# Kernel tuning notes

Hardware: AMD Instinct MI355X
Metric: run time of the kernel (lower is better)

Reference implementation:

```python
import jax, jax.numpy as jnp
import numpy as np

B, IN_DIM, OUT_DIM, N_KNOTS = 8192, 1024, 1024, 4


def setup_inputs() -> dict:
    key = jax.random.key(0)
    k_feat, k_phase, k_w = jax.random.split(key, 3)
    feats = jax.random.normal(k_feat, (B, IN_DIM), dtype=jnp.float32)
    phase = jax.random.uniform(k_phase, (B, 1), dtype=jnp.float32)  # phase in [0,1)
    x = jnp.concatenate([feats, phase], axis=1)  # [B, IN_DIM+1]
    bound = np.sqrt(6.0 / (OUT_DIM * IN_DIM))
    weight_knots = jax.random.uniform(
        k_w, (N_KNOTS, OUT_DIM, IN_DIM), dtype=jnp.float32, minval=-bound, maxval=bound)
    bias_knots = jnp.zeros((N_KNOTS, OUT_DIM), dtype=jnp.float32)
    return {"x": x, "weight_knots": weight_knots, "bias_knots": bias_knots}


def _cubic(y, mu):
    # Catmull-Rom cubic blend over the 4 gathered knots, y: [B,4,D], mu: [B,1]
    y0, y1, y2, y3 = y[:, 0], y[:, 1], y[:, 2], y[:, 3]
    return ((-0.5 * y0 + 1.5 * y1 - 1.5 * y2 + 0.5 * y3) * mu * mu * mu
            + (y0 - 2.5 * y1 + 2.0 * y2 - 0.5 * y3) * mu * mu
            + (-0.5 * y0 + 0.5 * y2) * mu + y1)


def reference(x, weight_knots, bias_knots):
    K = weight_knots.shape[0]
    phase = x[:, -1]            # [B]
    feats = x[:, :-1]           # [B, IN_DIM]
    pscale = K * phase
    mu = jnp.mod(pscale, 1.0)[:, None]                       # [B, 1]
    i1 = jnp.mod(pscale.astype(jnp.int32), K)
    idx = jnp.stack([jnp.mod(i1 - 1, K), i1,
                     jnp.mod(i1 + 1, K), jnp.mod(i1 + 2, K)], axis=1)  # [B, 4]
    # Exploit linearity: matvec against each knot matrix once, then blend.
    # Mathematically identical to cubic(W0,..,W3) @ feats + cubic(b0,..,b3).
    yk = jnp.einsum('koi,bi->bko', weight_knots, feats)      # [B, K, OUT]
    y4 = jnp.take_along_axis(yk, idx[:, :, None], axis=1)    # [B, 4, OUT]
    b4 = bias_knots[idx]                                     # [B, 4, OUT]
    res = _cubic(y4 + b4, mu)                                # cubic is linear in y
    return jax.nn.elu(res)
```

## Files before the change

kernel.cpp:

```cpp
#include <hip/hip_runtime.h>
#include <math.h>

#define IN_DIM 1024
#define OUT_DIM 1024
#define NROWS 8192
#define XSTRIDE 1025

typedef __attribute__((ext_vector_type(8))) short bf16x8;
typedef __attribute__((ext_vector_type(4))) float f32x4;

static __device__ __forceinline__ unsigned f2bf(float f) {
  union { float f; unsigned u; } v; v.f = f;
  unsigned u = v.u;
  return (u + 0x7fffu + ((u >> 16) & 1u)) >> 16;
}

__global__ __launch_bounds__(256) void prep_kernel(
    const float* __restrict__ x, const float* __restrict__ W,
    unsigned short* __restrict__ Wb, unsigned short* __restrict__ F,
    float* __restrict__ coef)
{
  const int blk = blockIdx.x;
  if (blk < 2048) {
    const int t = blk * 256 + threadIdx.x;
    const int flat = t * 8;
    const int k = flat >> 20;
    const int o = (flat >> 10) & 1023;
    const int i = flat & 1023;
    const float4 fa = *reinterpret_cast<const float4*>(W + flat);
    const float4 fb = *reinterpret_cast<const float4*>(W + flat + 4);
    uint4 pk;
    pk.x = f2bf(fa.x) | (f2bf(fa.y) << 16);
    pk.y = f2bf(fa.z) | (f2bf(fa.w) << 16);
    pk.z = f2bf(fb.x) | (f2bf(fb.y) << 16);
    pk.w = f2bf(fb.z) | (f2bf(fb.w) << 16);
    const int g = (o & 15) | (k << 4) | ((o >> 4) << 6);
    *reinterpret_cast<uint4*>(Wb + (size_t)g * 1024 + i) = pk;
  } else {
    const int b = blk - 2048;
    const float* xr = x + (size_t)b * XSTRIDE;
    const int i = threadIdx.x * 4;
    ushort4 vv;
    vv.x = (unsigned short)f2bf(xr[i]);     vv.y = (unsigned short)f2bf(xr[i + 1]);
    vv.z = (unsigned short)f2bf(xr[i + 2]); vv.w = (unsigned short)f2bf(xr[i + 3]);
    *reinterpret_cast<ushort4*>(F + (size_t)b * 1024 + i) = vv;
    if (threadIdx.x == 0) {
      const float ps = 4.0f * xr[IN_DIM];
      const int ip = (int)ps;
      const int i1 = ip & 3;
      const float mu = ps - (float)ip;
      const float mu2 = mu * mu, mu3 = mu2 * mu;
      const float c0 = -0.5f * mu3 +        mu2 - 0.5f * mu;
      const float c1 =  1.5f * mu3 - 2.5f * mu2 + 1.0f;
      const float c2 = -1.5f * mu3 + 2.0f * mu2 + 0.5f * mu;
      const float c3 =  0.5f * mu3 - 0.5f * mu2;
      const int d0 = (0-i1)&3, d1 = (1-i1)&3, d2 = (2-i1)&3, d3 = (3-i1)&3;
      float4 cv;
      cv.x = d0==0 ? c1 : d0==1 ? c2 : d0==2 ? c3 : c0;
      cv.y = d1==0 ? c1 : d1==1 ? c2 : d1==2 ? c3 : c0;
      cv.z = d2==0 ? c1 : d2==1 ? c2 : d2==2 ? c3 : c0;
      cv.w = d3==0 ? c1 : d3==1 ? c2 : d3==2 ? c3 : c0;
      *reinterpret_cast<float4*>(coef + (size_t)b * 4) = cv;
    }
  }
}

#define BM 256
#define BN 128
#define BK 64

__global__ __launch_bounds__(256, 2) void gemm_kernel(
    const unsigned short* __restrict__ F,
    const unsigned short* __restrict__ Wb,
    const float* __restrict__ coef,
    const float* __restrict__ bias,
    float* __restrict__ out)
{
  __shared__ unsigned short As[BM * BK];
  __shared__ unsigned short Bs[BN * BK];

  const int tid  = threadIdx.x;
  const int wave = tid >> 6;
  const int lane = tid & 63;
  const int row0  = blockIdx.y * BM;
  const int col0g = blockIdx.x * BN;

  const int srow = tid >> 3;
  const int scc  = tid & 7;
  const int sgc  = (scc ^ (srow & 7)) * 8;

  const int wr = (wave >> 1) * 128;
  const int wc = (wave & 1) * 64;
  const int fm = lane & 15;
  const int fq = lane >> 4;

  f32x4 acc[8][4];
  const f32x4 zero = {0.f, 0.f, 0.f, 0.f};
  #pragma unroll
  for (int a = 0; a < 8; a++)
    #pragma unroll
    for (int b = 0; b < 4; b++)
      acc[a][b] = zero;

  const unsigned short* Abase = F  + (size_t)row0  * 1024;
  const unsigned short* Bbase = Wb + (size_t)col0g * 1024;

  for (int kb = 0; kb < 1024; kb += BK) {
    #pragma unroll
    for (int it = 0; it < 8; it++) {
      const int r = srow + it * 32;
      __builtin_amdgcn_global_load_lds(
          (const __attribute__((address_space(1))) void*)(Abase + (size_t)r * 1024 + kb + sgc),
          (__attribute__((address_space(3))) void*)(As + r * BK + scc * 8), 16, 0, 0);
    }
    #pragma unroll
    for (int it = 0; it < 4; it++) {
      const int r = srow + it * 32;
      __builtin_amdgcn_global_load_lds(
          (const __attribute__((address_space(1))) void*)(Bbase + (size_t)r * 1024 + kb + sgc),
          (__attribute__((address_space(3))) void*)(Bs + r * BK + scc * 8), 16, 0, 0);
    }
    __syncthreads();

    #pragma unroll
    for (int kk = 0; kk < BK; kk += 32) {
      bf16x8 af[8], bfr[4];
      #pragma unroll
      for (int mi = 0; mi < 8; mi++) {
        const int r  = wr + mi * 16 + fm;
        const int lc = ((kk >> 3) + fq) ^ (fm & 7);
        af[mi] = *reinterpret_cast<const bf16x8*>(As + r * BK + lc * 8);
      }
      #pragma unroll
      for (int ni = 0; ni < 4; ni++) {
        const int r  = wc + ni * 16 + fm;
        const int lc = ((kk >> 3) + fq) ^ (fm & 7);
        bfr[ni] = *reinterpret_cast<const bf16x8*>(Bs + r * BK + lc * 8);
      }
      #pragma unroll
      for (int mi = 0; mi < 8; mi++)
        #pragma unroll
        for (int ni = 0; ni < 4; ni++)
          acc[mi][ni] = __builtin_amdgcn_mfma_f32_16x16x32_bf16(
              af[mi], bfr[ni], acc[mi][ni], 0, 0, 0);
    }
    __syncthreads();
  }

  const int o = fm + 16 * (2 * blockIdx.x + (wave & 1));
  const float b0 = bias[o];
  const float b1 = bias[OUT_DIM + o];
  const float b2 = bias[2 * OUT_DIM + o];
  const float b3 = bias[3 * OUT_DIM + o];
  #pragma unroll
  for (int mi = 0; mi < 8; mi++) {
    #pragma unroll
    for (int r = 0; r < 4; r++) {
      const int rloc = wr + mi * 16 + (fq << 2) + r;
      const float4 c = *reinterpret_cast<const float4*>(coef + (size_t)(row0 + rloc) * 4);
      float v = c.x * (acc[mi][0][r] + b0)
              + c.y * (acc[mi][1][r] + b1)
              + c.z * (acc[mi][2][r] + b2)
              + c.w * (acc[mi][3][r] + b3);
      const float e = __expf(v) - 1.0f;
      v = (v > 0.0f) ? v : e;
      out[(size_t)(row0 + rloc) * OUT_DIM + o] = v;
    }
  }
}

extern "C" void kernel_launch(void* const* d_in, const int* in_sizes, int n_in,
                              void* d_out, int out_size, void* d_ws, size_t ws_size,
                              hipStream_t stream) {
  const float* x  = (const float*)d_in[0];
  const float* wk = (const float*)d_in[1];
  const float* bk = (const float*)d_in[2];
  float* out = (float*)d_out;

  char* ws = (char*)d_ws;
  unsigned short* Wb = (unsigned short*)ws;
  unsigned short* F  = (unsigned short*)(ws + (8u << 20));
  float* coef        = (float*)(ws + (24u << 20));

  hipLaunchKernelGGL(prep_kernel, dim3(2048 + NROWS), dim3(256), 0, stream,
                     x, wk, Wb, F, coef);
  hipLaunchKernelGGL(gemm_kernel, dim3(4096 / BN, NROWS / BM), dim3(256), 0, stream,
                     F, Wb, coef, bk, out);
}
```

Before: 156.3 us.

## Switch GEMM to 32x32x16 bf16 MFMA with matching weight interleave

Replaces the 16x16x32 MFMA tiling with 32x32x16 MFMA instructions. Each wave now owns 64 rows by the full 128-column block, and the four knots of 32 outputs are interleaved per 32-column group. The weight prep layout changes from 16-output groups to 32-output groups so the knot blend stays within one lane's registers. The aim is fewer LDS fragment loads per MFMA and higher per-instruction throughput, at the cost of different register pressure and epilogue indexing.

```diff
diff --git a/kernel.cpp b/kernel.cpp
--- a/kernel.cpp
+++ b/kernel.cpp
@@ -7,7 +7,7 @@
 #define XSTRIDE 1025
 
 typedef __attribute__((ext_vector_type(8))) short bf16x8;
-typedef __attribute__((ext_vector_type(4))) float f32x4;
+typedef __attribute__((ext_vector_type(16))) float f32x16;
 
 static __device__ __forceinline__ unsigned f2bf(float f) {
   union { float f; unsigned u; } v; v.f = f;
@@ -34,7 +34,7 @@
     pk.y = f2bf(fa.z) | (f2bf(fa.w) << 16);
     pk.z = f2bf(fb.x) | (f2bf(fb.y) << 16);
     pk.w = f2bf(fb.z) | (f2bf(fb.w) << 16);
-    const int g = (o & 15) | (k << 4) | ((o >> 4) << 6);
+    const int g = (o & 31) | (k << 5) | ((o >> 5) << 7);
     *reinterpret_cast<uint4*>(Wb + (size_t)g * 1024 + i) = pk;
   } else {
     const int b = blk - 2048;
@@ -89,18 +89,16 @@
   const int scc  = tid & 7;
   const int sgc  = (scc ^ (srow & 7)) * 8;
 
-  const int wr = (wave >> 1) * 128;
-  const int wc = (wave & 1) * 64;
-  const int fm = lane & 15;
-  const int fq = lane >> 4;
+  const int wr = wave * 64;
+  const int lm = lane & 31;
+  const int hi = lane >> 5;
 
-  f32x4 acc[8][4];
-  const f32x4 zero = {0.f, 0.f, 0.f, 0.f};
+  f32x16 acc[2][4];
   #pragma unroll
-  for (int a = 0; a < 8; a++)
+  for (int a = 0; a < 2; a++)
     #pragma unroll
     for (int b = 0; b < 4; b++)
-      acc[a][b] = zero;
+      acc[a][b] = (f32x16)(0.0f);
 
   const unsigned short* Abase = F  + (size_t)row0  * 1024;
   const unsigned short* Bbase = Wb + (size_t)col0g * 1024;
@@ -123,45 +121,40 @@
     __syncthreads();
 
     #pragma unroll
-    for (int kk = 0; kk < BK; kk += 32) {
-      bf16x8 af[8], bfr[4];
+    for (int ks = 0; ks < 4; ks++) {
+      const int lc = ((2 * ks + hi) ^ (lm & 7)) * 8;
+      bf16x8 a[2], b[4];
       #pragma unroll
-      for (int mi = 0; mi < 8; mi++) {
-        const int r  = wr + mi * 16 + fm;
-        const int lc = ((kk >> 3) + fq) ^ (fm & 7);
-        af[mi] = *reinterpret_cast<const bf16x8*>(As + r * BK + lc * 8);
-      }
+      for (int mi = 0; mi < 2; mi++)
+        a[mi] = *reinterpret_cast<const bf16x8*>(As + (wr + mi * 32 + lm) * BK + lc);
       #pragma unroll
-      for (int ni = 0; ni < 4; ni++) {
-        const int r  = wc + ni * 16 + fm;
-        const int lc = ((kk >> 3) + fq) ^ (fm & 7);
-        bfr[ni] = *reinterpret_cast<const bf16x8*>(Bs + r * BK + lc * 8);
-      }
+      for (int nj = 0; nj < 4; nj++)
+        b[nj] = *reinterpret_cast<const bf16x8*>(Bs + (nj * 32 + lm) * BK + lc);
       #pragma unroll
-      for (int mi = 0; mi < 8; mi++)
+      for (int mi = 0; mi < 2; mi++)
         #pragma unroll
-        for (int ni = 0; ni < 4; ni++)
-          acc[mi][ni] = __builtin_amdgcn_mfma_f32_16x16x32_bf16(
-              af[mi], bfr[ni], acc[mi][ni], 0, 0, 0);
+        for (int nj = 0; nj < 4; nj++)
+          acc[mi][nj] = __builtin_amdgcn_mfma_f32_32x32x16_bf16(
+              a[mi], b[nj], acc[mi][nj], 0, 0, 0);
     }
     __syncthreads();
   }
 
-  const int o = fm + 16 * (2 * blockIdx.x + (wave & 1));
+  const int o = (blockIdx.x << 5) + lm;
   const float b0 = bias[o];
   const float b1 = bias[OUT_DIM + o];
   const float b2 = bias[2 * OUT_DIM + o];
   const float b3 = bias[3 * OUT_DIM + o];
   #pragma unroll
-  for (int mi = 0; mi < 8; mi++) {
+  for (int mi = 0; mi < 2; mi++) {
     #pragma unroll
-    for (int r = 0; r < 4; r++) {
-      const int rloc = wr + mi * 16 + (fq << 2) + r;
+    for (int reg = 0; reg < 16; reg++) {
+      const int rloc = wr + mi * 32 + (reg & 3) + 8 * (reg >> 2) + 4 * hi;
       const float4 c = *reinterpret_cast<const float4*>(coef + (size_t)(row0 + rloc) * 4);
-      float v = c.x * (acc[mi][0][r] + b0)
-              + c.y * (acc[mi][1][r] + b1)
-              + c.z * (acc[mi][2][r] + b2)
-              + c.w * (acc[mi][3][r] + b3);
+      float v = c.x * (acc[mi][0][reg] + b0)
+              + c.y * (acc[mi][1][reg] + b1)
+              + c.z * (acc[mi][2][reg] + b2)
+              + c.w * (acc[mi][3][reg] + b3);
       const float e = __expf(v) - 1.0f;
       v = (v > 0.0f) ? v : e;
       out[(size_t)(row0 + rloc) * OUT_DIM + o] = v;
```

Result: slower. 164.0 us (+4.9%).
